# Optimization experiments

Hardware: AMD Instinct MI355X
Metric: run time of the kernel (lower is better)

The kernel has to match this reference:

```python
import jax, jax.numpy as jnp
import numpy as np

BS, NS, NSTEP = 128, 1024, 8
IN_DIM, HID, MLP = 768, 512, 512
NEG = -100000.0


def setup_inputs() -> dict:
    key = jax.random.key(0)
    ks = jax.random.split(key, 12)
    s_h = 1.0 / np.sqrt(HID)
    s_cat = 1.0 / np.sqrt(HID + IN_DIM)
    s_m = 1.0 / np.sqrt(MLP)
    # gumbel noise implements Categorical sampling as argmax(logits + gumbel)
    u = jax.random.uniform(ks[9], (NSTEP, BS, NS), jnp.float32, 1e-7, 1.0 - 1e-7)
    return {
        "target_emb": jax.random.normal(ks[0], (BS, IN_DIM), jnp.float32),
        "ctx_emb": jax.random.normal(ks[1], (BS, NS, IN_DIM), jnp.float32),
        "target_len": jax.random.randint(ks[2], (BS,), 1, 32),
        "ctx_len": jax.random.randint(ks[3], (BS,), NSTEP, NS + 1),
        "n_step": NSTEP,
        "W_ih": jax.random.normal(ks[4], (4 * HID, IN_DIM), jnp.float32) * s_h,
        "W_hh": jax.random.normal(ks[5], (4 * HID, HID), jnp.float32) * s_h,
        "b_ih": jnp.zeros((4 * HID,), jnp.float32),
        "b_hh": jnp.zeros((4 * HID,), jnp.float32),
        "W1c": jax.random.normal(ks[6], (MLP, IN_DIM), jnp.float32) * s_cat,
        "W1h": jax.random.normal(ks[7], (MLP, HID), jnp.float32) * s_cat,
        "b1": jnp.zeros((MLP,), jnp.float32),
        "w2": jax.random.normal(ks[8], (MLP,), jnp.float32) * s_m,
        "b2": jnp.zeros((), jnp.float32),
        "gumbel": -jnp.log(-jnp.log(u)),
    }


def reference(target_emb, ctx_emb, target_len, ctx_len, n_step,
              W_ih, W_hh, b_ih, b_hh, W1c, W1h, b1, w2, b2, gumbel):
    bs, ns, in_dim = ctx_emb.shape
    hid = W_hh.shape[1]
    # mlp1 split: ctx part is constant across steps (concat([ctx, h]) @ W1^T = ctx@W1c^T + h@W1h^T)
    ctx_part = jnp.einsum('bnd,md->bnm', ctx_emb, W1c) + b1  # [bs, ns, mlp]
    mask0 = jnp.where(jnp.arange(ns)[None, :] >= ctx_len[:, None], NEG, 0.0).astype(jnp.float32)
    h0 = jnp.zeros((bs, hid), jnp.float32)
    c0 = jnp.zeros((bs, hid), jnp.float32)
    lp0 = jnp.zeros((bs,), jnp.float32)
    batch_idx = jnp.arange(bs)

    def step(carry, g):
        h, c, mask, x, lp = carry
        # LSTMCell (torch gate order: i, f, g, o); dropout is identity (eval semantics)
        gates = x @ W_ih.T + b_ih + h @ W_hh.T + b_hh
        i_g, f_g, g_g, o_g = jnp.split(gates, 4, axis=-1)
        c_new = jax.nn.sigmoid(f_g) * c + jax.nn.sigmoid(i_g) * jnp.tanh(g_g)
        h_new = jax.nn.sigmoid(o_g) * jnp.tanh(c_new)
        # attention-style MLP score
        pre = ctx_part + (h_new @ W1h.T)[:, None, :]          # [bs, ns, mlp]
        sc = jnp.tanh(pre) @ w2 + b2 + mask                   # [bs, ns]
        # Categorical(probs=softmax(sc)).sample() via Gumbel-argmax
        out = jnp.argmax(sc + g, axis=-1)                     # [bs]
        lp = lp + jnp.take_along_axis(jax.nn.log_softmax(sc, axis=-1), out[:, None], 1)[:, 0]
        mask = mask.at[batch_idx, out].set(NEG)
        x_new = jnp.take_along_axis(ctx_emb, out[:, None, None], axis=1)[:, 0, :]
        return (h_new, c_new, mask, x_new, lp), out

    (h, c, mask, x, log_probs), outputs = jax.lax.scan(
        step, (h0, c0, mask0, target_emb, lp0), gumbel)
    return outputs, log_probs
```

## Files before the change

kernel.cpp:

```cpp
#include <hip/hip_runtime.h>
#include <hip/hip_bf16.h>

#define BSZ 128
#define NSQ 1024
#define NSTEPC 8
#define IND 768
#define HIDD 512
#define G4D 2048
#define MLPD 512
#define KXD 1280
#define NEGV -100000.0f
#define KSG 16
#define KSH 8
#define MSPLIT 4

typedef __attribute__((ext_vector_type(4))) float f32x4;
typedef __attribute__((ext_vector_type(8))) short short8v;

__device__ __forceinline__ float bf2f(unsigned short u) {
  unsigned int x = ((unsigned int)u) << 16;
  return __builtin_bit_cast(float, x);
}

__device__ __forceinline__ float tanh_fast(float x) {
  x = fminf(fmaxf(x, -15.0f), 15.0f);
  float e = __builtin_amdgcn_exp2f(x * 2.8853900817779268f);
  float r = __builtin_amdgcn_rcpf(e + 1.0f);
  return fmaf(-2.0f, r, 1.0f);
}

__global__ __launch_bounds__(256) void k_init(
    const float* __restrict__ te, const int* __restrict__ cl,
    float* __restrict__ mask, float* __restrict__ xh,
    float* __restrict__ cst, float* __restrict__ lp) {
  const int b = blockIdx.x, tid = threadIdx.x;
  const int L = cl[b];
  for (int n = tid; n < NSQ; n += 256) mask[(size_t)b*NSQ + n] = (n >= L) ? NEGV : 0.0f;
  for (int d = tid; d < IND; d += 256) xh[(size_t)b*KXD + d] = te[(size_t)b*IND + d];
  for (int j = tid; j < HIDD; j += 256) {
    xh[(size_t)b*KXD + IND + j] = 0.0f;
    cst[(size_t)b*HIDD + j] = 0.0f;
  }
  if (tid == 0) lp[b] = 0.0f;
}

__global__ __launch_bounds__(256) void k_ctx_mfma(
    const float* __restrict__ A,
    const float* __restrict__ W,
    const float* __restrict__ bias,
    const int* __restrict__ clen,
    float* __restrict__ cp) {
  __shared__ short sCh[128*32], sCl[128*32], sWh[128*32], sWl[128*32];
  __shared__ float sb1[128];
  const int m0 = blockIdx.x * 128;
  const int i0 = blockIdx.y * 128;
  const int b = i0 >> 10;
  const int nbase = i0 & 1023;
  if (nbase >= clen[b]) return;
  const int tid = threadIdx.x;
  if (tid < 128) sb1[tid] = bias[m0 + tid];
  const int lane = tid & 63;
  const int wid = tid >> 6;
  const int wm = wid & 1, wn = wid >> 1;
  const int l15 = lane & 15, l4 = lane >> 4;

  f32x4 acc[4][4] = {};

  for (int k0 = 0; k0 < IND; k0 += 32) {
#pragma unroll
    for (int u = 0; u < 2; ++u) {
      const int c = tid + u * 256;
      const int row = c >> 2, kcs = c & 3;
      const int kread = kcs ^ ((row >> 1) & 3);
      const int off = row * 32 + kcs * 8;
      {
        const float* s = W + (size_t)(m0 + row) * IND + k0 + kread * 8;
        const float4 f0 = *(const float4*)s, f1 = *(const float4*)(s + 4);
        const float fv[8] = {f0.x, f0.y, f0.z, f0.w, f1.x, f1.y, f1.z, f1.w};
        short8v hi, lo;
#pragma unroll
        for (int j = 0; j < 8; ++j) {
          const unsigned int ub = __builtin_bit_cast(unsigned int, fv[j]);
          const unsigned int hb = ub & 0xFFFF0000u;
          const float lf = fv[j] - __builtin_bit_cast(float, hb);
          hi[j] = (short)(hb >> 16);
          lo[j] = (short)(__builtin_bit_cast(unsigned int, lf) >> 16);
        }
        *(short8v*)&sWh[off] = hi;
        *(short8v*)&sWl[off] = lo;
      }
      {
        const float* s = A + (size_t)(i0 + row) * IND + k0 + kread * 8;
        const float4 f0 = *(const float4*)s, f1 = *(const float4*)(s + 4);
        const float fv[8] = {f0.x, f0.y, f0.z, f0.w, f1.x, f1.y, f1.z, f1.w};
        short8v hi, lo;
#pragma unroll
        for (int j = 0; j < 8; ++j) {
          const unsigned int ub = __builtin_bit_cast(unsigned int, fv[j]);
          const unsigned int hb = ub & 0xFFFF0000u;
          const float lf = fv[j] - __builtin_bit_cast(float, hb);
          hi[j] = (short)(hb >> 16);
          lo[j] = (short)(__builtin_bit_cast(unsigned int, lf) >> 16);
        }
        *(short8v*)&sCh[off] = hi;
        *(short8v*)&sCl[off] = lo;
      }
    }
    __syncthreads();
    short8v wh[4], wl[4], chv[4], clv[4];
#pragma unroll
    for (int f = 0; f < 4; ++f) {
      const int rw = wm * 64 + f * 16 + l15;
      const int offw = rw * 32 + ((l4 ^ ((rw >> 1) & 3)) << 3);
      wh[f] = *(const short8v*)&sWh[offw];
      wl[f] = *(const short8v*)&sWl[offw];
      const int rc = wn * 64 + f * 16 + l15;
      const int offc = rc * 32 + ((l4 ^ ((rc >> 1) & 3)) << 3);
      chv[f] = *(const short8v*)&sCh[offc];
      clv[f] = *(const short8v*)&sCl[offc];
    }
#pragma unroll
    for (int fm = 0; fm < 4; ++fm)
#pragma unroll
      for (int fn = 0; fn < 4; ++fn) {
        acc[fm][fn] = __builtin_amdgcn_mfma_f32_16x16x32_bf16(wh[fm], chv[fn], acc[fm][fn], 0, 0, 0);
        acc[fm][fn] = __builtin_amdgcn_mfma_f32_16x16x32_bf16(wh[fm], clv[fn], acc[fm][fn], 0, 0, 0);
        acc[fm][fn] = __builtin_amdgcn_mfma_f32_16x16x32_bf16(wl[fm], chv[fn], acc[fm][fn], 0, 0, 0);
      }
    __syncthreads();
  }
#pragma unroll
  for (int fm = 0; fm < 4; ++fm) {
#pragma unroll
    for (int r = 0; r < 4; ++r) {
      const int m = m0 + wm * 64 + fm * 16 + l4 * 4 + r;
      const float bb = sb1[m - m0];
      float* dst = cp + (((size_t)(b * MLPD + m)) << 10) + nbase + wn * 64 + l15;
#pragma unroll
      for (int fn = 0; fn < 4; ++fn)
        dst[fn * 16] = acc[fm][fn][r] + bb;
    }
  }
}

__global__ __launch_bounds__(256) void k_pgemm(
    const float* __restrict__ A, int lda, int acol,
    const float* __restrict__ B0, int ldb0, int kb,
    const float* __restrict__ B1, int ldb1,
    int kTiles, int N, float* __restrict__ P) {
  __shared__ float As[16][128];
  __shared__ float Bs[16][132];
  const int n0 = blockIdx.x * 128;
  const int kc0 = blockIdx.y * kTiles * 16;
  const int tid = threadIdx.x;
  const int tn = tid & 15;
  const int ta = tid >> 4;
  float acc[8][8] = {};
  for (int t = 0; t < kTiles; ++t) {
    const int k0 = kc0 + t * 16;
#pragma unroll
    for (int u = 0; u < 2; ++u) {
      const int v = tid + u * 256;
      const int r = v >> 2, kc = v & 3;
      const float4 a4 = *(const float4*)(A + (size_t)r * lda + acol + k0 + kc * 4);
      As[kc*4+0][r] = a4.x; As[kc*4+1][r] = a4.y; As[kc*4+2][r] = a4.z; As[kc*4+3][r] = a4.w;
      const float* bp = (k0 < kb) ? (B0 + (size_t)(n0 + r) * ldb0 + k0 + kc * 4)
                                  : (B1 + (size_t)(n0 + r) * ldb1 + (k0 - kb) + kc * 4);
      const float4 b4 = *(const float4*)bp;
      Bs[kc*4+0][r] = b4.x; Bs[kc*4+1][r] = b4.y; Bs[kc*4+2][r] = b4.z; Bs[kc*4+3][r] = b4.w;
    }
    __syncthreads();
#pragma unroll
    for (int kk = 0; kk < 16; ++kk) {
      float av[8], bv[8];
#pragma unroll
      for (int q = 0; q < 8; ++q) av[q] = As[kk][ta*8+q];
#pragma unroll
      for (int q = 0; q < 8; ++q) bv[q] = Bs[kk][tn*8+q];
#pragma unroll
      for (int ri = 0; ri < 8; ++ri)
#pragma unroll
        for (int ni = 0; ni < 8; ++ni)
          acc[ri][ni] = fmaf(av[ri], bv[ni], acc[ri][ni]);
    }
    __syncthreads();
  }
#pragma unroll
  for (int ri = 0; ri < 8; ++ri) {
    const int i = ta * 8 + ri;
    float* p = P + ((size_t)blockIdx.y * BSZ + i) * N + n0 + tn * 8;
    *(float4*)(p + 0) = make_float4(acc[ri][0], acc[ri][1], acc[ri][2], acc[ri][3]);
    *(float4*)(p + 4) = make_float4(acc[ri][4], acc[ri][5], acc[ri][6], acc[ri][7]);
  }
}

__global__ __launch_bounds__(512) void k_lstm(
    const float* __restrict__ gp, const float* __restrict__ b_ih,
    const float* __restrict__ b_hh, float* __restrict__ cst, float* __restrict__ xh) {
  const int b = blockIdx.x, j = threadIdx.x;
  float g[4];
#pragma unroll
  for (int q = 0; q < 4; ++q) {
    float s = b_ih[q*HIDD + j] + b_hh[q*HIDD + j];
#pragma unroll
    for (int ks = 0; ks < KSG; ++ks) s += gp[((size_t)ks*BSZ + b)*G4D + q*HIDD + j];
    g[q] = s;
  }
  const float c_old = cst[(size_t)b*HIDD + j];
  const float ig = 1.0f / (1.0f + expf(-g[0]));
  const float fg = 1.0f / (1.0f + expf(-g[1]));
  const float gg = tanhf(g[2]);
  const float og = 1.0f / (1.0f + expf(-g[3]));
  const float cn = fg * c_old + ig * gg;
  const float hn = og * tanhf(cn);
  cst[(size_t)b*HIDD + j] = cn;
  xh[(size_t)b*KXD + IND + j] = hn;
}

__global__ __launch_bounds__(256) void k_scores(
    const float* __restrict__ cp, const float* __restrict__ hpp,
    const float* __restrict__ w2, const int* __restrict__ clen,
    float* __restrict__ psc) {
  const int mh = blockIdx.x;
  const int b = blockIdx.y;
  const int tid = threadIdx.x;
  __shared__ float hs[128], ws[128];
  if (tid < 128) {
    const int m = mh * 128 + tid;
    float s = 0.0f;
#pragma unroll
    for (int ks = 0; ks < KSH; ++ks) s += hpp[((size_t)ks*BSZ + b)*MLPD + m];
    hs[tid] = s;
    ws[tid] = w2[m];
  }
  __syncthreads();
  const int len = clen[b];
  const int n0 = tid * 4;
  if (n0 >= len) return;
  float ax = 0, ay = 0, az = 0, aw = 0;
  const float* base = cp + ((size_t)b * MLPD + mh * 128) * NSQ + n0;
#pragma unroll 4
  for (int mm = 0; mm < 128; ++mm) {
    const float4 c4 = *(const float4*)(base + (size_t)mm * NSQ);
    const float h = hs[mm], w = ws[mm];
    ax = fmaf(tanh_fast(c4.x + h), w, ax);
    ay = fmaf(tanh_fast(c4.y + h), w, ay);
    az = fmaf(tanh_fast(c4.z + h), w, az);
    aw = fmaf(tanh_fast(c4.w + h), w, aw);
  }
  *(float4*)(psc + ((size_t)b * MSPLIT + mh) * NSQ + n0) = make_float4(ax, ay, az, aw);
}

__global__ __launch_bounds__(256) void k_argmax(
    const float* __restrict__ psc, float* __restrict__ mask,
    const float* __restrict__ gum, const float* __restrict__ b2p,
    float* __restrict__ lp, const float* __restrict__ ctx,
    float* __restrict__ xh, float* __restrict__ outv, int step) {
  const int b = blockIdx.x, tid = threadIdx.x;
  __shared__ float rv[256], rs[256], rm[256];
  __shared__ int ri[256];
  __shared__ int sel;
  const float b2 = b2p[0];
  const int n0 = tid * 4;
  const float4 m4 = *(const float4*)(mask + (size_t)b * NSQ + n0);
  float sc[4] = {b2 + m4.x, b2 + m4.y, b2 + m4.z, b2 + m4.w};
#pragma unroll
  for (int mh = 0; mh < MSPLIT; ++mh) {
    const float4 p4 = *(const float4*)(psc + ((size_t)b * MSPLIT + mh) * NSQ + n0);
    sc[0] += p4.x; sc[1] += p4.y; sc[2] += p4.z; sc[3] += p4.w;
  }
  const float4 g4 = *(const float4*)(gum + ((size_t)step * BSZ + b) * NSQ + n0);
  const float gv[4] = {g4.x, g4.y, g4.z, g4.w};
  float bestv = -1e30f, bests = 0.0f, msc = -1e30f;
  int bestn = 0;
#pragma unroll
  for (int q = 0; q < 4; ++q) {
    const float v = sc[q] + gv[q];
    if (v > bestv) { bestv = v; bestn = n0 + q; bests = sc[q]; }
    msc = fmaxf(msc, sc[q]);
  }
  rv[tid] = bestv; ri[tid] = bestn; rs[tid] = bests; rm[tid] = msc;
  __syncthreads();
  for (int o = 128; o > 0; o >>= 1) {
    if (tid < o) {
      if (rv[tid+o] > rv[tid] || (rv[tid+o] == rv[tid] && ri[tid+o] < ri[tid])) {
        rv[tid] = rv[tid+o]; ri[tid] = ri[tid+o]; rs[tid] = rs[tid+o];
      }
      rm[tid] = fmaxf(rm[tid], rm[tid+o]);
    }
    __syncthreads();
  }
  const float M = rm[0];
  __syncthreads();
  float se = 0.0f;
#pragma unroll
  for (int q = 0; q < 4; ++q)
    se += __builtin_amdgcn_exp2f((sc[q] - M) * 1.4426950408889634f);
  rm[tid] = se;
  __syncthreads();
  for (int o = 128; o > 0; o >>= 1) {
    if (tid < o) rm[tid] += rm[tid+o];
    __syncthreads();
  }
  if (tid == 0) {
    const int n = ri[0];
    const float lse = M + logf(rm[0]);
    const float nlp = lp[b] + rs[0] - lse;
    lp[b] = nlp;
    mask[(size_t)b * NSQ + n] = NEGV;
    outv[step * BSZ + b] = (float)n;
    if (step == NSTEPC - 1) outv[NSTEPC * BSZ + b] = nlp;
    sel = n;
  }
  __syncthreads();
  const int n = sel;
  const float4* src = (const float4*)(ctx + ((size_t)b * NSQ + n) * IND);
  float4* dst = (float4*)(xh + (size_t)b * KXD);
  for (int d = tid; d < IND / 4; d += 256) dst[d] = src[d];
}

extern "C" void kernel_launch(void* const* d_in, const int* in_sizes, int n_in,
                              void* d_out, int out_size, void* d_ws, size_t ws_size,
                              hipStream_t stream) {
  const float* target_emb = (const float*)d_in[0];
  const float* ctx_emb   = (const float*)d_in[1];
  const int*   ctx_len   = (const int*)d_in[3];
  const float* W_ih = (const float*)d_in[5];
  const float* W_hh = (const float*)d_in[6];
  const float* b_ih = (const float*)d_in[7];
  const float* b_hh = (const float*)d_in[8];
  const float* W1c  = (const float*)d_in[9];
  const float* W1h  = (const float*)d_in[10];
  const float* b1   = (const float*)d_in[11];
  const float* w2   = (const float*)d_in[12];
  const float* b2   = (const float*)d_in[13];
  const float* gumbel = (const float*)d_in[14];
  float* out = (float*)d_out;

  float* ws = (float*)d_ws;
  size_t off = 0;
  auto alloc = [&](size_t n) { float* p = ws + off; off += (n + 63) & ~(size_t)63; return p; };

  float* cp   = alloc((size_t)BSZ * MLPD * NSQ);
  float* gp   = alloc((size_t)KSG * BSZ * G4D);
  float* hpp  = alloc((size_t)KSH * BSZ * MLPD);
  float* psc  = alloc((size_t)BSZ * MSPLIT * NSQ);
  float* mask = alloc((size_t)BSZ * NSQ);
  float* xh   = alloc((size_t)BSZ * KXD);
  float* cst  = alloc((size_t)BSZ * HIDD);
  float* lp   = alloc(128);

  k_init<<<BSZ, 256, 0, stream>>>(target_emb, ctx_len, mask, xh, cst, lp);

  k_ctx_mfma<<<dim3(MLPD/128, (BSZ*NSQ)/128), 256, 0, stream>>>(
      ctx_emb, W1c, b1, ctx_len, cp);

  for (int t = 0; t < NSTEPC; ++t) {
    k_pgemm<<<dim3(G4D/128, KSG), 256, 0, stream>>>(
        xh, KXD, 0, W_ih, IND, IND, W_hh, HIDD, 5, G4D, gp);
    k_lstm<<<BSZ, 512, 0, stream>>>(gp, b_ih, b_hh, cst, xh);
    k_pgemm<<<dim3(MLPD/128, KSH), 256, 0, stream>>>(
        xh, KXD, IND, W1h, HIDD, 1 << 30, nullptr, 0, 4, MLPD, hpp);
    k_scores<<<dim3(MSPLIT, BSZ), 256, 0, stream>>>(cp, hpp, w2, ctx_len, psc);
    k_argmax<<<BSZ, 256, 0, stream>>>(psc, mask, gumbel, b2, lp, ctx_emb, xh, out, t);
  }
}
```

Measured before the change: 909.2 us.

## Pre-split weights to bf16 hi/lo tiles and use MFMA for LSTM gates

Weights W1c, W_ih and W_hh are converted once into pre-swizzled bf16 hi/lo tile planes, so the ctx GEMM and a new MFMA gate GEMM can stream them into LDS with global_load_lds instead of converting fp32 on every tile. The LSTM input vector is kept as bf16 hi/lo planes written directly by the init, LSTM and argmax kernels. The h@W1h projection is fused into the LSTM kernel as a per-thread dot product, which removes one GEMM launch per step and its split-K reduction. The ctx GEMM retiles to 256x64 blocks. The gate GEMM uses split-K 4 instead of 16. The costs are an extra prep kernel and a three-term bf16 split accuracy approximation in the gate GEMM.

```diff
diff --git a/kernel.cpp b/kernel.cpp
--- a/kernel.cpp
+++ b/kernel.cpp
@@ -8,18 +8,29 @@
 #define HIDD 512
 #define G4D 2048
 #define MLPD 512
-#define KXD 1280
 #define NEGV -100000.0f
-#define KSG 16
-#define KSH 8
+#define KSGATE 4
 #define MSPLIT 4
 
 typedef __attribute__((ext_vector_type(4))) float f32x4;
 typedef __attribute__((ext_vector_type(8))) short short8v;
 
-__device__ __forceinline__ float bf2f(unsigned short u) {
-  unsigned int x = ((unsigned int)u) << 16;
-  return __builtin_bit_cast(float, x);
+__device__ __forceinline__ void gl16(const unsigned short* g, unsigned short* l) {
+  __builtin_amdgcn_global_load_lds(
+      (const __attribute__((address_space(1))) unsigned int*)(g),
+      (__attribute__((address_space(3))) unsigned int*)(l), 16, 0, 0);
+}
+
+__device__ __forceinline__ void split2(float4 f0, float4 f1, short8v& hi, short8v& lo) {
+  float fv[8] = {f0.x, f0.y, f0.z, f0.w, f1.x, f1.y, f1.z, f1.w};
+#pragma unroll
+  for (int j = 0; j < 8; ++j) {
+    const unsigned ub = __builtin_bit_cast(unsigned, fv[j]);
+    const unsigned hb = ub & 0xFFFF0000u;
+    const float lf = fv[j] - __builtin_bit_cast(float, hb);
+    hi[j] = (short)(hb >> 16);
+    lo[j] = (short)(__builtin_bit_cast(unsigned, lf) >> 16);
+  }
 }
 
 __device__ __forceinline__ float tanh_fast(float x) {
@@ -29,113 +40,135 @@
   return fmaf(-2.0f, r, 1.0f);
 }
 
-__global__ __launch_bounds__(256) void k_init(
+__global__ __launch_bounds__(256) void k_prep_w(
+    const float* __restrict__ W1c, const float* __restrict__ W_ih,
+    const float* __restrict__ W_hh,
+    unsigned short* __restrict__ wch, unsigned short* __restrict__ wcl,
+    unsigned short* __restrict__ wgh, unsigned short* __restrict__ wgl) {
+  int c = blockIdx.x * 256 + threadIdx.x;
+  const float* src;
+  unsigned short *dh, *dl;
+  size_t unit;
+  if (c < 49152) {
+    const int row = c / 96, wc = c - row * 96;
+    const int tile = wc >> 2, c4 = wc & 3;
+    const int slot = c4 ^ ((row >> 1) & 3);
+    unit = ((size_t)((row >> 7) * 24 + tile) * 128 + (row & 127)) * 4 + slot;
+    src = W1c + (size_t)row * IND + wc * 8;
+    dh = wch; dl = wcl;
+  } else {
+    c -= 49152;
+    if (c >= 327680) return;
+    const int row = c / 160, wc = c - row * 160;
+    const int k0 = wc * 8;
+    const int tile = wc >> 2, c4 = wc & 3;
+    const int slot = c4 ^ ((row >> 1) & 3);
+    unit = ((size_t)((row >> 7) * 40 + tile) * 128 + (row & 127)) * 4 + slot;
+    src = (k0 < IND) ? (W_ih + (size_t)row * IND + k0)
+                     : (W_hh + (size_t)row * HIDD + (k0 - IND));
+    dh = wgh; dl = wgl;
+  }
+  const float4 f0 = *(const float4*)src, f1 = *(const float4*)(src + 4);
+  short8v hi, lo;
+  split2(f0, f1, hi, lo);
+  *(short8v*)(dh + unit * 8) = hi;
+  *(short8v*)(dl + unit * 8) = lo;
+}
+
+__global__ __launch_bounds__(256) void k_init2(
     const float* __restrict__ te, const int* __restrict__ cl,
-    float* __restrict__ mask, float* __restrict__ xh,
-    float* __restrict__ cst, float* __restrict__ lp) {
+    float* __restrict__ mask, float* __restrict__ cst, float* __restrict__ lp,
+    unsigned short* __restrict__ xhh, unsigned short* __restrict__ xhl) {
   const int b = blockIdx.x, tid = threadIdx.x;
   const int L = cl[b];
-  for (int n = tid; n < NSQ; n += 256) mask[(size_t)b*NSQ + n] = (n >= L) ? NEGV : 0.0f;
-  for (int d = tid; d < IND; d += 256) xh[(size_t)b*KXD + d] = te[(size_t)b*IND + d];
-  for (int j = tid; j < HIDD; j += 256) {
-    xh[(size_t)b*KXD + IND + j] = 0.0f;
-    cst[(size_t)b*HIDD + j] = 0.0f;
-  }
+  for (int n = tid; n < NSQ; n += 256) mask[(size_t)b * NSQ + n] = (n >= L) ? NEGV : 0.0f;
+  for (int j = tid; j < HIDD; j += 256) cst[(size_t)b * HIDD + j] = 0.0f;
   if (tid == 0) lp[b] = 0.0f;
-}
-
-__global__ __launch_bounds__(256) void k_ctx_mfma(
-    const float* __restrict__ A,
-    const float* __restrict__ W,
-    const float* __restrict__ bias,
-    const int* __restrict__ clen,
+  if (tid < 160) {
+    const int tile = tid >> 2, c4 = tid & 3;
+    const int slot = c4 ^ ((b >> 1) & 3);
+    const size_t ub = (((size_t)tile * 128 + b) * 4 + slot) * 8;
+    short8v hi = {}, lo = {};
+    if (tid < 96) {
+      const float* s = te + (size_t)b * IND + tid * 8;
+      split2(*(const float4*)s, *(const float4*)(s + 4), hi, lo);
+    }
+    *(short8v*)&xhh[ub] = hi;
+    *(short8v*)&xhl[ub] = lo;
+  }
+}
+
+__global__ __launch_bounds__(256) void k_ctx2(
+    const float* __restrict__ ctx,
+    const unsigned short* __restrict__ wch, const unsigned short* __restrict__ wcl,
+    const float* __restrict__ bias, const int* __restrict__ clen,
     float* __restrict__ cp) {
-  __shared__ short sCh[128*32], sCl[128*32], sWh[128*32], sWl[128*32];
-  __shared__ float sb1[128];
-  const int m0 = blockIdx.x * 128;
-  const int i0 = blockIdx.y * 128;
+  __shared__ __align__(16) unsigned short sWh[8192], sWl[8192];
+  __shared__ __align__(16) unsigned short sCh[2048], sCl[2048];
+  const int i0 = blockIdx.y * 64;
   const int b = i0 >> 10;
   const int nbase = i0 & 1023;
   if (nbase >= clen[b]) return;
+  const int m0 = blockIdx.x * 256;
+  const int rb0 = blockIdx.x * 2;
   const int tid = threadIdx.x;
-  if (tid < 128) sb1[tid] = bias[m0 + tid];
-  const int lane = tid & 63;
-  const int wid = tid >> 6;
-  const int wm = wid & 1, wn = wid >> 1;
+  const int lane = tid & 63, wid = tid >> 6;
   const int l15 = lane & 15, l4 = lane >> 4;
+  const int crow = tid >> 2, cc4 = tid & 3;
+  const int ckread = cc4 ^ ((crow >> 1) & 3);
+  const float* csrc = ctx + (size_t)(i0 + crow) * IND + ckread * 8;
 
   f32x4 acc[4][4] = {};
-
-  for (int k0 = 0; k0 < IND; k0 += 32) {
-#pragma unroll
-    for (int u = 0; u < 2; ++u) {
-      const int c = tid + u * 256;
-      const int row = c >> 2, kcs = c & 3;
-      const int kread = kcs ^ ((row >> 1) & 3);
-      const int off = row * 32 + kcs * 8;
-      {
-        const float* s = W + (size_t)(m0 + row) * IND + k0 + kread * 8;
-        const float4 f0 = *(const float4*)s, f1 = *(const float4*)(s + 4);
-        const float fv[8] = {f0.x, f0.y, f0.z, f0.w, f1.x, f1.y, f1.z, f1.w};
-        short8v hi, lo;
-#pragma unroll
-        for (int j = 0; j < 8; ++j) {
-          const unsigned int ub = __builtin_bit_cast(unsigned int, fv[j]);
-          const unsigned int hb = ub & 0xFFFF0000u;
-          const float lf = fv[j] - __builtin_bit_cast(float, hb);
-          hi[j] = (short)(hb >> 16);
-          lo[j] = (short)(__builtin_bit_cast(unsigned int, lf) >> 16);
-        }
-        *(short8v*)&sWh[off] = hi;
-        *(short8v*)&sWl[off] = lo;
+  for (int t = 0; t < 24; ++t) {
+#pragma unroll
+    for (int i = 0; i < 8; ++i) {
+      const int v = wid * 1024 + i * 4096;
+      const int plane = v >> 14;
+      const int rem = v & 16383;
+      const int rbh = rem >> 13;
+      const int offs = (rem & 8191) >> 1;
+      const unsigned short* g = (plane ? wcl : wch) +
+          ((size_t)((rb0 + rbh) * 24 + t)) * 4096 + offs + lane * 8;
+      unsigned short* l = (plane ? sWl : sWh) + rbh * 4096 + offs;
+      gl16(g, l);
+    }
+    {
+      const float* s = csrc + t * 32;
+      short8v hi, lo;
+      split2(*(const float4*)s, *(const float4*)(s + 4), hi, lo);
+      *(short8v*)&sCh[tid * 8] = hi;
+      *(short8v*)&sCl[tid * 8] = lo;
+    }
+    __syncthreads();
+    short8v ah[4], al[4], bh[4], bl[4];
+#pragma unroll
+    for (int f = 0; f < 4; ++f) {
+      const int rw = wid * 64 + f * 16 + l15;
+      const int sw = l4 ^ ((rw >> 1) & 3);
+      ah[f] = *(const short8v*)&sWh[rw * 32 + sw * 8];
+      al[f] = *(const short8v*)&sWl[rw * 32 + sw * 8];
+      const int rc = f * 16 + l15;
+      const int sc = l4 ^ ((rc >> 1) & 3);
+      bh[f] = *(const short8v*)&sCh[rc * 32 + sc * 8];
+      bl[f] = *(const short8v*)&sCl[rc * 32 + sc * 8];
+    }
+#pragma unroll
+    for (int fm = 0; fm < 4; ++fm)
+#pragma unroll
+      for (int fn = 0; fn < 4; ++fn) {
+        acc[fm][fn] = __builtin_amdgcn_mfma_f32_16x16x32_bf16(ah[fm], bh[fn], acc[fm][fn], 0, 0, 0);
+        acc[fm][fn] = __builtin_amdgcn_mfma_f32_16x16x32_bf16(ah[fm], bl[fn], acc[fm][fn], 0, 0, 0);
+        acc[fm][fn] = __builtin_amdgcn_mfma_f32_16x16x32_bf16(al[fm], bh[fn], acc[fm][fn], 0, 0, 0);
       }
-      {
-        const float* s = A + (size_t)(i0 + row) * IND + k0 + kread * 8;
-        const float4 f0 = *(const float4*)s, f1 = *(const float4*)(s + 4);
-        const float fv[8] = {f0.x, f0.y, f0.z, f0.w, f1.x, f1.y, f1.z, f1.w};
-        short8v hi, lo;
-#pragma unroll
-        for (int j = 0; j < 8; ++j) {
-          const unsigned int ub = __builtin_bit_cast(unsigned int, fv[j]);
-          const unsigned int hb = ub & 0xFFFF0000u;
-          const float lf = fv[j] - __builtin_bit_cast(float, hb);
-          hi[j] = (short)(hb >> 16);
-          lo[j] = (short)(__builtin_bit_cast(unsigned int, lf) >> 16);
-        }
-        *(short8v*)&sCh[off] = hi;
-        *(short8v*)&sCl[off] = lo;
-      }
-    }
-    __syncthreads();
-    short8v wh[4], wl[4], chv[4], clv[4];
-#pragma unroll
-    for (int f = 0; f < 4; ++f) {
-      const int rw = wm * 64 + f * 16 + l15;
-      const int offw = rw * 32 + ((l4 ^ ((rw >> 1) & 3)) << 3);
-      wh[f] = *(const short8v*)&sWh[offw];
-      wl[f] = *(const short8v*)&sWl[offw];
-      const int rc = wn * 64 + f * 16 + l15;
-      const int offc = rc * 32 + ((l4 ^ ((rc >> 1) & 3)) << 3);
-      chv[f] = *(const short8v*)&sCh[offc];
-      clv[f] = *(const short8v*)&sCl[offc];
-    }
-#pragma unroll
-    for (int fm = 0; fm < 4; ++fm)
-#pragma unroll
-      for (int fn = 0; fn < 4; ++fn) {
-        acc[fm][fn] = __builtin_amdgcn_mfma_f32_16x16x32_bf16(wh[fm], chv[fn], acc[fm][fn], 0, 0, 0);
-        acc[fm][fn] = __builtin_amdgcn_mfma_f32_16x16x32_bf16(wh[fm], clv[fn], acc[fm][fn], 0, 0, 0);
-        acc[fm][fn] = __builtin_amdgcn_mfma_f32_16x16x32_bf16(wl[fm], chv[fn], acc[fm][fn], 0, 0, 0);
-      }
     __syncthreads();
   }
 #pragma unroll
   for (int fm = 0; fm < 4; ++fm) {
 #pragma unroll
     for (int r = 0; r < 4; ++r) {
-      const int m = m0 + wm * 64 + fm * 16 + l4 * 4 + r;
-      const float bb = sb1[m - m0];
-      float* dst = cp + (((size_t)(b * MLPD + m)) << 10) + nbase + wn * 64 + l15;
+      const int m = m0 + wid * 64 + fm * 16 + l4 * 4 + r;
+      const float bb = bias[m];
+      float* dst = cp + (((size_t)(b * MLPD + m)) << 10) + nbase + l15;
 #pragma unroll
       for (int fn = 0; fn < 4; ++fn)
         dst[fn * 16] = acc[fm][fn][r] + bb;
@@ -143,78 +176,115 @@
   }
 }
 
-__global__ __launch_bounds__(256) void k_pgemm(
-    const float* __restrict__ A, int lda, int acol,
-    const float* __restrict__ B0, int ldb0, int kb,
-    const float* __restrict__ B1, int ldb1,
-    int kTiles, int N, float* __restrict__ P) {
-  __shared__ float As[16][128];
-  __shared__ float Bs[16][132];
-  const int n0 = blockIdx.x * 128;
-  const int kc0 = blockIdx.y * kTiles * 16;
+__global__ __launch_bounds__(256) void k_gates(
+    const unsigned short* __restrict__ xhh, const unsigned short* __restrict__ xhl,
+    const unsigned short* __restrict__ wgh, const unsigned short* __restrict__ wgl,
+    float* __restrict__ gp) {
+  __shared__ __align__(16) unsigned short sAh[4096], sAl[4096], sBh[4096], sBl[4096];
+  const int nb = blockIdx.x;
+  const int ks = blockIdx.y;
   const int tid = threadIdx.x;
-  const int tn = tid & 15;
-  const int ta = tid >> 4;
-  float acc[8][8] = {};
-  for (int t = 0; t < kTiles; ++t) {
-    const int k0 = kc0 + t * 16;
-#pragma unroll
-    for (int u = 0; u < 2; ++u) {
-      const int v = tid + u * 256;
-      const int r = v >> 2, kc = v & 3;
-      const float4 a4 = *(const float4*)(A + (size_t)r * lda + acol + k0 + kc * 4);
-      As[kc*4+0][r] = a4.x; As[kc*4+1][r] = a4.y; As[kc*4+2][r] = a4.z; As[kc*4+3][r] = a4.w;
-      const float* bp = (k0 < kb) ? (B0 + (size_t)(n0 + r) * ldb0 + k0 + kc * 4)
-                                  : (B1 + (size_t)(n0 + r) * ldb1 + (k0 - kb) + kc * 4);
-      const float4 b4 = *(const float4*)bp;
-      Bs[kc*4+0][r] = b4.x; Bs[kc*4+1][r] = b4.y; Bs[kc*4+2][r] = b4.z; Bs[kc*4+3][r] = b4.w;
-    }
-    __syncthreads();
-#pragma unroll
-    for (int kk = 0; kk < 16; ++kk) {
-      float av[8], bv[8];
-#pragma unroll
-      for (int q = 0; q < 8; ++q) av[q] = As[kk][ta*8+q];
-#pragma unroll
-      for (int q = 0; q < 8; ++q) bv[q] = Bs[kk][tn*8+q];
-#pragma unroll
-      for (int ri = 0; ri < 8; ++ri)
-#pragma unroll
-        for (int ni = 0; ni < 8; ++ni)
-          acc[ri][ni] = fmaf(av[ri], bv[ni], acc[ri][ni]);
-    }
-    __syncthreads();
-  }
-#pragma unroll
-  for (int ri = 0; ri < 8; ++ri) {
-    const int i = ta * 8 + ri;
-    float* p = P + ((size_t)blockIdx.y * BSZ + i) * N + n0 + tn * 8;
-    *(float4*)(p + 0) = make_float4(acc[ri][0], acc[ri][1], acc[ri][2], acc[ri][3]);
-    *(float4*)(p + 4) = make_float4(acc[ri][4], acc[ri][5], acc[ri][6], acc[ri][7]);
-  }
-}
-
-__global__ __launch_bounds__(512) void k_lstm(
+  const int lane = tid & 63, wid = tid >> 6;
+  const int wm = wid >> 1, wn = wid & 1;
+  const int l15 = lane & 15, l4 = lane >> 4;
+  f32x4 acc[4][4] = {};
+  for (int t = 0; t < 10; ++t) {
+    const int gt = ks * 10 + t;
+#pragma unroll
+    for (int i = 0; i < 8; ++i) {
+      const int v = wid * 1024 + i * 4096;
+      const int mm = v >> 13;
+      const int offs = (v & 8191) >> 1;
+      const unsigned short* g;
+      unsigned short* l;
+      if (mm == 0)      { g = xhh + (size_t)gt * 4096 + offs; l = sAh + offs; }
+      else if (mm == 1) { g = xhl + (size_t)gt * 4096 + offs; l = sAl + offs; }
+      else if (mm == 2) { g = wgh + ((size_t)nb * 40 + gt) * 4096 + offs; l = sBh + offs; }
+      else              { g = wgl + ((size_t)nb * 40 + gt) * 4096 + offs; l = sBl + offs; }
+      gl16(g + lane * 8, l);
+    }
+    __syncthreads();
+    short8v ahv[4], alv[4], bhv[4], blv[4];
+#pragma unroll
+    for (int f = 0; f < 4; ++f) {
+      const int ri = wm * 64 + f * 16 + l15;
+      const int sa = l4 ^ ((ri >> 1) & 3);
+      ahv[f] = *(const short8v*)&sAh[ri * 32 + sa * 8];
+      alv[f] = *(const short8v*)&sAl[ri * 32 + sa * 8];
+      const int rn = wn * 64 + f * 16 + l15;
+      const int sb = l4 ^ ((rn >> 1) & 3);
+      bhv[f] = *(const short8v*)&sBh[rn * 32 + sb * 8];
+      blv[f] = *(const short8v*)&sBl[rn * 32 + sb * 8];
+    }
+#pragma unroll
+    for (int fi = 0; fi < 4; ++fi)
+#pragma unroll
+      for (int fn = 0; fn < 4; ++fn) {
+        acc[fi][fn] = __builtin_amdgcn_mfma_f32_16x16x32_bf16(ahv[fi], bhv[fn], acc[fi][fn], 0, 0, 0);
+        acc[fi][fn] = __builtin_amdgcn_mfma_f32_16x16x32_bf16(ahv[fi], blv[fn], acc[fi][fn], 0, 0, 0);
+        acc[fi][fn] = __builtin_amdgcn_mfma_f32_16x16x32_bf16(alv[fi], bhv[fn], acc[fi][fn], 0, 0, 0);
+      }
+    __syncthreads();
+  }
+#pragma unroll
+  for (int fi = 0; fi < 4; ++fi) {
+#pragma unroll
+    for (int r = 0; r < 4; ++r) {
+      const int i = wm * 64 + fi * 16 + l4 * 4 + r;
+      float* dst = gp + ((size_t)ks * BSZ + i) * G4D + nb * 128 + wn * 64 + l15;
+#pragma unroll
+      for (int fn = 0; fn < 4; ++fn)
+        dst[fn * 16] = acc[fi][fn][r];
+    }
+  }
+}
+
+__global__ __launch_bounds__(512) void k_lstm2(
     const float* __restrict__ gp, const float* __restrict__ b_ih,
-    const float* __restrict__ b_hh, float* __restrict__ cst, float* __restrict__ xh) {
+    const float* __restrict__ b_hh, const float* __restrict__ W1h,
+    float* __restrict__ cst,
+    unsigned short* __restrict__ xhh, unsigned short* __restrict__ xhl,
+    float* __restrict__ hpp) {
+  __shared__ float hs[HIDD];
   const int b = blockIdx.x, j = threadIdx.x;
   float g[4];
 #pragma unroll
   for (int q = 0; q < 4; ++q) {
-    float s = b_ih[q*HIDD + j] + b_hh[q*HIDD + j];
-#pragma unroll
-    for (int ks = 0; ks < KSG; ++ks) s += gp[((size_t)ks*BSZ + b)*G4D + q*HIDD + j];
+    float s = b_ih[q * HIDD + j] + b_hh[q * HIDD + j];
+#pragma unroll
+    for (int ks = 0; ks < KSGATE; ++ks)
+      s += gp[((size_t)ks * BSZ + b) * G4D + q * HIDD + j];
     g[q] = s;
   }
-  const float c_old = cst[(size_t)b*HIDD + j];
+  const float c_old = cst[(size_t)b * HIDD + j];
   const float ig = 1.0f / (1.0f + expf(-g[0]));
   const float fg = 1.0f / (1.0f + expf(-g[1]));
   const float gg = tanhf(g[2]);
   const float og = 1.0f / (1.0f + expf(-g[3]));
   const float cn = fg * c_old + ig * gg;
   const float hn = og * tanhf(cn);
-  cst[(size_t)b*HIDD + j] = cn;
-  xh[(size_t)b*KXD + IND + j] = hn;
+  cst[(size_t)b * HIDD + j] = cn;
+  hs[j] = hn;
+  {
+    const int tile = 24 + (j >> 5);
+    const int c4 = (j >> 3) & 3;
+    const int slot = c4 ^ ((b >> 1) & 3);
+    const size_t u16i = (((size_t)tile * 128 + b) * 4 + slot) * 8 + (j & 7);
+    const unsigned ubh = __builtin_bit_cast(unsigned, hn) & 0xFFFF0000u;
+    const float lf = hn - __builtin_bit_cast(float, ubh);
+    xhh[u16i] = (unsigned short)(ubh >> 16);
+    xhl[u16i] = (unsigned short)(__builtin_bit_cast(unsigned, lf) >> 16);
+  }
+  __syncthreads();
+  const float* wr = W1h + (size_t)j * HIDD;
+  float s = 0.0f;
+#pragma unroll 4
+  for (int k = 0; k < HIDD; k += 4) {
+    const float4 h4 = *(const float4*)&hs[k];
+    const float4 w4 = *(const float4*)&wr[k];
+    s = fmaf(h4.x, w4.x, fmaf(h4.y, w4.y, fmaf(h4.z, w4.z, fmaf(h4.w, w4.w, s))));
+  }
+  hpp[(size_t)b * HIDD + j] = s;
 }
 
 __global__ __launch_bounds__(256) void k_scores(
@@ -224,14 +294,10 @@
   const int mh = blockIdx.x;
   const int b = blockIdx.y;
   const int tid = threadIdx.x;
-  __shared__ float hs[128], ws[128];
+  __shared__ float hsm[128], wsm[128];
   if (tid < 128) {
-    const int m = mh * 128 + tid;
-    float s = 0.0f;
-#pragma unroll
-    for (int ks = 0; ks < KSH; ++ks) s += hpp[((size_t)ks*BSZ + b)*MLPD + m];
-    hs[tid] = s;
-    ws[tid] = w2[m];
+    hsm[tid] = hpp[(size_t)b * MLPD + mh * 128 + tid];
+    wsm[tid] = w2[mh * 128 + tid];
   }
   __syncthreads();
   const int len = clen[b];
@@ -242,7 +308,7 @@
 #pragma unroll 4
   for (int mm = 0; mm < 128; ++mm) {
     const float4 c4 = *(const float4*)(base + (size_t)mm * NSQ);
-    const float h = hs[mm], w = ws[mm];
+    const float h = hsm[mm], w = wsm[mm];
     ax = fmaf(tanh_fast(c4.x + h), w, ax);
     ay = fmaf(tanh_fast(c4.y + h), w, ay);
     az = fmaf(tanh_fast(c4.z + h), w, az);
@@ -255,7 +321,8 @@
     const float* __restrict__ psc, float* __restrict__ mask,
     const float* __restrict__ gum, const float* __restrict__ b2p,
     float* __restrict__ lp, const float* __restrict__ ctx,
-    float* __restrict__ xh, float* __restrict__ outv, int step) {
+    unsigned short* __restrict__ xhh, unsigned short* __restrict__ xhl,
+    float* __restrict__ outv, int step) {
   const int b = blockIdx.x, tid = threadIdx.x;
   __shared__ float rv[256], rs[256], rm[256];
   __shared__ int ri[256];
@@ -283,10 +350,10 @@
   __syncthreads();
   for (int o = 128; o > 0; o >>= 1) {
     if (tid < o) {
-      if (rv[tid+o] > rv[tid] || (rv[tid+o] == rv[tid] && ri[tid+o] < ri[tid])) {
-        rv[tid] = rv[tid+o]; ri[tid] = ri[tid+o]; rs[tid] = rs[tid+o];
+      if (rv[tid + o] > rv[tid] || (rv[tid + o] == rv[tid] && ri[tid + o] < ri[tid])) {
+        rv[tid] = rv[tid + o]; ri[tid] = ri[tid + o]; rs[tid] = rs[tid + o];
       }
-      rm[tid] = fmaxf(rm[tid], rm[tid+o]);
+      rm[tid] = fmaxf(rm[tid], rm[tid + o]);
     }
     __syncthreads();
   }
@@ -299,7 +366,7 @@
   rm[tid] = se;
   __syncthreads();
   for (int o = 128; o > 0; o >>= 1) {
-    if (tid < o) rm[tid] += rm[tid+o];
+    if (tid < o) rm[tid] += rm[tid + o];
     __syncthreads();
   }
   if (tid == 0) {
@@ -314,9 +381,16 @@
   }
   __syncthreads();
   const int n = sel;
-  const float4* src = (const float4*)(ctx + ((size_t)b * NSQ + n) * IND);
-  float4* dst = (float4*)(xh + (size_t)b * KXD);
-  for (int d = tid; d < IND / 4; d += 256) dst[d] = src[d];
+  if (tid < 96) {
+    const float* src = ctx + ((size_t)b * NSQ + n) * IND + tid * 8;
+    const int tile = tid >> 2, c4 = tid & 3;
+    const int slot = c4 ^ ((b >> 1) & 3);
+    const size_t ub = (((size_t)tile * 128 + b) * 4 + slot) * 8;
+    short8v hi, lo;
+    split2(*(const float4*)src, *(const float4*)(src + 4), hi, lo);
+    *(short8v*)&xhh[ub] = hi;
+    *(short8v*)&xhl[ub] = lo;
+  }
 }
 
 extern "C" void kernel_launch(void* const* d_in, const int* in_sizes, int n_in,
@@ -342,26 +416,27 @@
   auto alloc = [&](size_t n) { float* p = ws + off; off += (n + 63) & ~(size_t)63; return p; };
 
   float* cp   = alloc((size_t)BSZ * MLPD * NSQ);
-  float* gp   = alloc((size_t)KSG * BSZ * G4D);
-  float* hpp  = alloc((size_t)KSH * BSZ * MLPD);
+  float* gp   = alloc((size_t)KSGATE * BSZ * G4D);
+  float* hpp  = alloc((size_t)BSZ * MLPD);
   float* psc  = alloc((size_t)BSZ * MSPLIT * NSQ);
   float* mask = alloc((size_t)BSZ * NSQ);
-  float* xh   = alloc((size_t)BSZ * KXD);
   float* cst  = alloc((size_t)BSZ * HIDD);
   float* lp   = alloc(128);
-
-  k_init<<<BSZ, 256, 0, stream>>>(target_emb, ctx_len, mask, xh, cst, lp);
-
-  k_ctx_mfma<<<dim3(MLPD/128, (BSZ*NSQ)/128), 256, 0, stream>>>(
-      ctx_emb, W1c, b1, ctx_len, cp);
+  unsigned short* wch = (unsigned short*)alloc(196608);
+  unsigned short* wcl = (unsigned short*)alloc(196608);
+  unsigned short* wgh = (unsigned short*)alloc(1310720);
+  unsigned short* wgl = (unsigned short*)alloc(1310720);
+  unsigned short* xhh = (unsigned short*)alloc(81920);
+  unsigned short* xhl = (unsigned short*)alloc(81920);
+
+  k_prep_w<<<1472, 256, 0, stream>>>(W1c, W_ih, W_hh, wch, wcl, wgh, wgl);
+  k_init2<<<BSZ, 256, 0, stream>>>(target_emb, ctx_len, mask, cst, lp, xhh, xhl);
+  k_ctx2<<<dim3(2, 2048), 256, 0, stream>>>(ctx_emb, wch, wcl, b1, ctx_len, cp);
 
   for (int t = 0; t < NSTEPC; ++t) {
-    k_pgemm<<<dim3(G4D/128, KSG), 256, 0, stream>>>(
-        xh, KXD, 0, W_ih, IND, IND, W_hh, HIDD, 5, G4D, gp);
-    k_lstm<<<BSZ, 512, 0, stream>>>(gp, b_ih, b_hh, cst, xh);
-    k_pgemm<<<dim3(MLPD/128, KSH), 256, 0, stream>>>(
-        xh, KXD, IND, W1h, HIDD, 1 << 30, nullptr, 0, 4, MLPD, hpp);
+    k_gates<<<dim3(16, KSGATE), 256, 0, stream>>>(xhh, xhl, wgh, wgl, gp);
+    k_lstm2<<<BSZ, 512, 0, stream>>>(gp, b_ih, b_hh, W1h, cst, xhh, xhl, hpp);
     k_scores<<<dim3(MSPLIT, BSZ), 256, 0, stream>>>(cp, hpp, w2, ctx_len, psc);
-    k_argmax<<<BSZ, 256, 0, stream>>>(psc, mask, gumbel, b2, lp, ctx_emb, xh, out, t);
-  }
-}
+    k_argmax<<<BSZ, 256, 0, stream>>>(psc, mask, gumbel, b2, lp, ctx_emb, xhh, xhl, out, t);
+  }
+}
```

New measurement: 953.8 us. +4.9%, slower.
